# Kernel tuning notes

Hardware: AMD Instinct MI355X
Metric: run time of the kernel (lower is better)

Reference implementation:

```python
import jax, jax.numpy as jnp
import numpy as np

D_MODEL = 1024
N_HEAD = 16
DK = D_MODEL // N_HEAD
D_FF = 2048
EPS = 1e-6
NEG = -1e10


def layer_norm(x, gamma, beta):
    # torch .std() is unbiased (N-1), and eps is added to std (not var)
    mean = jnp.mean(x, axis=-1, keepdims=True)
    var = jnp.sum((x - mean) ** 2, axis=-1, keepdims=True) / (x.shape[-1] - 1)
    std = jnp.sqrt(var)
    return gamma * (x - mean) / (std + EPS) + beta


def setup_inputs() -> dict:
    key = jax.random.key(0)
    ks = jax.random.split(key, 12)
    s = 0.02
    inp = {
        'x': jax.random.normal(ks[0], (16, 512, D_MODEL), dtype=jnp.float32),
        'x_mask': jax.random.randint(ks[1], (16, 1, 1, 512), 0, 2, dtype=jnp.int32),
        'Wq': jax.random.normal(ks[2], (D_MODEL, D_MODEL), dtype=jnp.float32) * s,
        'bq': jnp.zeros((D_MODEL,), jnp.float32),
        'Wk': jax.random.normal(ks[3], (D_MODEL, D_MODEL), dtype=jnp.float32) * s,
        'bk': jnp.zeros((D_MODEL,), jnp.float32),
        'Wv': jax.random.normal(ks[4], (D_MODEL, D_MODEL), dtype=jnp.float32) * s,
        'bv': jnp.zeros((D_MODEL,), jnp.float32),
        'Wo': jax.random.normal(ks[5], (D_MODEL, D_MODEL), dtype=jnp.float32) * s,
        'bo': jnp.zeros((D_MODEL,), jnp.float32),
        'gamma1': jnp.ones((D_MODEL,), jnp.float32),
        'beta1': jnp.zeros((D_MODEL,), jnp.float32),
        'W1': jax.random.normal(ks[6], (D_MODEL, D_FF), dtype=jnp.float32) * s,
        'b1': jnp.zeros((D_FF,), jnp.float32),
        'W2': jax.random.normal(ks[7], (D_FF, D_MODEL), dtype=jnp.float32) * s,
        'b2': jnp.zeros((D_MODEL,), jnp.float32),
        'gamma2': jnp.ones((D_MODEL,), jnp.float32),
        'beta2': jnp.zeros((D_MODEL,), jnp.float32),
    }
    return inp


def reference(x, x_mask, Wq, bq, Wk, bk, Wv, bv, Wo, bo, gamma1, beta1,
              W1, b1, W2, b2, gamma2, beta2):
    B, S, _ = x.shape
    # QKV projections -> [B, S, H, DK]
    q = (x @ Wq + bq).reshape(B, S, N_HEAD, DK)
    k = (x @ Wk + bk).reshape(B, S, N_HEAD, DK)
    v = (x @ Wv + bv).reshape(B, S, N_HEAD, DK)
    # scores [B, H, Sq, Sk]
    scores = jnp.einsum('bqhd,bkhd->bhqk', q, k) / jnp.sqrt(jnp.float32(DK))
    scores = jnp.where(x_mask == 0, jnp.float32(NEG), scores)
    probs = jax.nn.softmax(scores, axis=-1)
    attn = jnp.einsum('bhqk,bkhd->bqhd', probs, v).reshape(B, S, D_MODEL)
    attn_out = attn @ Wo + bo
    # residual + post-LN 1
    h = layer_norm(attn_out + x, gamma1, beta1)
    # FFN (exact GELU as torch nn.GELU default)
    ffn = jax.nn.gelu(h @ W1 + b1, approximate=False) @ W2 + b2
    out = layer_norm(ffn + h, gamma2, beta2)
    return out
```

## Files before the change

### kernel.cpp

```cpp
#include <hip/hip_runtime.h>
#include <math.h>

#define B_ 16
#define S_ 512
#define DM 1024
#define NH 16
#define DFF 2048

typedef short bf16x8 __attribute__((ext_vector_type(8)));
typedef float f32x4 __attribute__((ext_vector_type(4)));
typedef unsigned short u16;

__device__ __forceinline__ u16 f2bf(float f) {
  unsigned int u = __float_as_uint(f);
  u += 0x7FFF + ((u >> 16) & 1);
  return (u16)(u >> 16);
}

__device__ __forceinline__ float bf2f(u16 u) {
  return __uint_as_float(((unsigned)u) << 16);
}

__device__ __forceinline__ unsigned cvtpk_bf16(float lo, float hi) {
  unsigned r;
  asm("v_cvt_pk_bf16_f32 %0, %1, %2" : "=v"(r) : "v"(lo), "v"(hi));
  return r;
}

__device__ __forceinline__ float gelu_exact(float x) {
  return 0.5f * x * (1.0f + erff(x * 0.70710678118654752f));
}

__device__ __forceinline__ void gload_lds16(const void* g, void* l) {
  __builtin_amdgcn_global_load_lds((const __attribute__((address_space(1))) void*)g,
                                   (__attribute__((address_space(3))) void*)l, 16, 0, 0);
}

#define QSCALE 0.18033688011112042f
#define MASKNEG -1.442695e10f


__global__ void cvt_bf16_k(const float* __restrict__ in, u16* __restrict__ out, int n) {
  int i = (blockIdx.x * blockDim.x + threadIdx.x) * 4;
  float4 v = *(const float4*)(in + i);
  uint2 pk;
  pk.x = (unsigned)f2bf(v.x) | ((unsigned)f2bf(v.y) << 16);
  pk.y = (unsigned)f2bf(v.z) | ((unsigned)f2bf(v.w) << 16);
  *(uint2*)(out + i) = pk;
}

__global__ void transpose_bf16(const float* __restrict__ W, u16* __restrict__ Wt, int K, int N) {
  __shared__ float tile[32][33];
  int n0 = blockIdx.x * 32, k0 = blockIdx.y * 32;
  int tx = threadIdx.x, ty = threadIdx.y;
#pragma unroll
  for (int j = 0; j < 32; j += 8)
    tile[ty + j][tx] = W[(size_t)(k0 + ty + j) * N + n0 + tx];
  __syncthreads();
#pragma unroll
  for (int j = 0; j < 32; j += 8)
    Wt[(size_t)(n0 + ty + j) * K + k0 + tx] = f2bf(tile[tx][ty + j]);
}

__global__ void bias_cat(const float* __restrict__ bq, const float* __restrict__ bk,
                         const float* __restrict__ bv, float* __restrict__ o) {
  int i = blockIdx.x * 256 + threadIdx.x;
  o[i] = (i < 1024) ? bq[i] : ((i < 2048) ? bk[i - 1024] : bv[i - 2048]);
}

template <int EPI>
__global__ __launch_bounds__(256, 2)
void gemm_mfma(const u16* __restrict__ A, const u16* __restrict__ Bt,
               const float* __restrict__ bias, void* __restrict__ Cout,
               u16* __restrict__ vT, int M, int N, int K) {
  __shared__ __align__(16) char lds[73728];
  const int tid = threadIdx.x;
  const int w = tid >> 6, lane = tid & 63;
  const int wm = w >> 1, wn = w & 1;

  const int gx = gridDim.x;
  const int nwg = gx * gridDim.y;
  const int lin = blockIdx.y * gx + blockIdx.x;
  const int wg = (lin & 7) * (nwg >> 3) + (lin >> 3);
  const int bm = wg / gx, bn = wg % gx;

  const int NT = K >> 5;

  const int srow = w * 16 + (lane >> 2);
  const int skel = ((lane & 3) ^ (lane >> 4)) * 8;
  const u16* gA = A + (size_t)(bm * 256 + srow) * K + skel;
  const u16* gB = Bt + (size_t)(bn * 128 + srow) * K + skel;
  const size_t rs64 = (size_t)64 * K;
  const int dstb = w * 1024;

  const int lr = lane & 15, kg = lane >> 4;
  const int kslot = (kg ^ ((lr >> 2) & 3)) << 4;
  const int fAoff = (wm * 128 + lr) * 64 + kslot;
  const int fBoff = 16384 + (wn * 64 + lr) * 64 + kslot;

  f32x4 acc[8][4];
#pragma unroll
  for (int i = 0; i < 8; ++i)
#pragma unroll
    for (int j = 0; j < 4; ++j) acc[i][j] = (f32x4){0.f, 0.f, 0.f, 0.f};

#define STAGE_A(t_, sl_)                                         \
  do {                                                           \
    const u16* g_ = gA + (size_t)(t_) * 32;                      \
    char* d_ = lds + (sl_) * 24576 + dstb;                       \
    gload_lds16(g_, d_);                                         \
    gload_lds16(g_ + rs64, d_ + 4096);                           \
    gload_lds16(g_ + 2 * rs64, d_ + 8192);                       \
    gload_lds16(g_ + 3 * rs64, d_ + 12288);                      \
  } while (0)
#define STAGE_B(t_, sl_)                                         \
  do {                                                           \
    const u16* g_ = gB + (size_t)(t_) * 32;                      \
    char* d_ = lds + (sl_) * 24576 + 16384 + dstb;               \
    gload_lds16(g_, d_);                                         \
    gload_lds16(g_ + rs64, d_ + 4096);                           \
  } while (0)

  STAGE_A(0, 0);
  STAGE_B(0, 0);
  STAGE_A(1, 1);
  STAGE_B(1, 1);
  asm volatile("s_waitcnt vmcnt(6)" ::: "memory");
  __builtin_amdgcn_s_barrier();
  __builtin_amdgcn_sched_barrier(0);

  int cs = 0, ss = 2;
  for (int t = 0; t < NT; ++t) {
    const int st = (t + 2 < NT) ? (t + 2) : (NT - 1);
    const char* fA = lds + cs * 24576 + fAoff;
    const char* fB = lds + cs * 24576 + fBoff;
    bf16x8 av[4], bv[4];
#pragma unroll
    for (int mi = 0; mi < 4; ++mi) av[mi] = *(const bf16x8*)(fA + mi * 1024);
#pragma unroll
    for (int ni = 0; ni < 4; ++ni) bv[ni] = *(const bf16x8*)(fB + ni * 1024);
    STAGE_A(st, ss);
    __builtin_amdgcn_s_setprio(1);
#pragma unroll
    for (int mi = 0; mi < 4; ++mi)
#pragma unroll
      for (int ni = 0; ni < 4; ++ni)
        acc[mi][ni] = __builtin_amdgcn_mfma_f32_16x16x32_bf16(av[mi], bv[ni], acc[mi][ni], 0, 0, 0);
    __builtin_amdgcn_s_setprio(0);
    bf16x8 av2[4];
#pragma unroll
    for (int mi = 0; mi < 4; ++mi) av2[mi] = *(const bf16x8*)(fA + 4096 + mi * 1024);
    STAGE_B(st, ss);
    __builtin_amdgcn_s_setprio(1);
#pragma unroll
    for (int mi = 0; mi < 4; ++mi)
#pragma unroll
      for (int ni = 0; ni < 4; ++ni)
        acc[4 + mi][ni] = __builtin_amdgcn_mfma_f32_16x16x32_bf16(av2[mi], bv[ni], acc[4 + mi][ni], 0, 0, 0);
    __builtin_amdgcn_s_setprio(0);
    asm volatile("s_waitcnt vmcnt(6) lgkmcnt(0)" ::: "memory");
    __builtin_amdgcn_s_barrier();
    __builtin_amdgcn_sched_barrier(0);
    cs = (cs == 2) ? 0 : cs + 1;
    ss = (ss == 2) ? 0 : ss + 1;
  }
#undef STAGE_A
#undef STAGE_B

  const int crow0 = bm * 256 + wm * 128;
  const int ccol0 = bn * 128 + wn * 64;
#pragma unroll
  for (int mi = 0; mi < 8; ++mi) {
#pragma unroll
    for (int ni = 0; ni < 4; ++ni) {
      const int col = ccol0 + ni * 16 + lr;
      const float bv = bias[col];
      const int rowb = crow0 + mi * 16 + (lane >> 4) * 4;
      float v[4];
#pragma unroll
      for (int r = 0; r < 4; ++r) v[r] = acc[mi][ni][r] + bv;
      if (EPI == 1) {
#pragma unroll
        for (int r = 0; r < 4; ++r)
          ((u16*)Cout)[(size_t)(rowb + r) * N + col] = f2bf(gelu_exact(v[r]));
      } else if (EPI == 2) {
#pragma unroll
        for (int r = 0; r < 4; ++r)
          ((float*)Cout)[(size_t)(rowb + r) * N + col] = v[r];
      } else if (EPI == 4) {
#pragma unroll
        for (int r = 0; r < 4; ++r)
          ((u16*)Cout)[(size_t)(rowb + r) * N + col] = f2bf(v[r]);
      } else {
        if (col < 2048) {
          const float sc = (col < 1024) ? QSCALE : 1.0f;
#pragma unroll
          for (int r = 0; r < 4; ++r)
            ((u16*)Cout)[(size_t)(rowb + r) * 2048 + col] = f2bf(v[r] * sc);
        } else {
          const int b = rowb >> 9, s = rowb & 511;
          const int hd = col - 2048;
          ushort4 pk;
          pk.x = f2bf(v[0]); pk.y = f2bf(v[1]); pk.z = f2bf(v[2]); pk.w = f2bf(v[3]);
          *(ushort4*)(vT + ((size_t)(b * NH + (hd >> 6)) * 64 + (hd & 63)) * S_ + s) = pk;
        }
      }
    }
  }
}

__global__ __launch_bounds__(256, 3)
void attn_kernel(const u16* __restrict__ qk,
                 const u16* __restrict__ vT,
                 const int* __restrict__ mask,
                 u16* __restrict__ out) {
  __shared__ __align__(16) u16 Qs[32 * 72];
  __shared__ __align__(16) u16 Pl[32 * 520];
  __shared__ __align__(16) float Mlf[512];
  __shared__ __align__(16) float Rsum[32][4];

  const int tid = threadIdx.x;
  const int w = tid >> 6, lane = tid & 63;
  const int bid = blockIdx.x;
  const int widx = (bid & 7) * 512 + (bid >> 3);
  const int qt = widx & 15, h = (widx >> 4) & 15, b = widx >> 8;
  const int q0 = qt * 32;
  const int arow = lane & 15, kg = lane >> 4;

  {
    int r = tid >> 3, slot = tid & 7;
    bf16x8 v = *(const bf16x8*)(qk + (size_t)(b * S_ + q0 + r) * 2048 + h * 64 + slot * 8);
    *(bf16x8*)((char*)Qs + r * 144 + slot * 16) = v;
  }
  Mlf[tid] = (mask[b * S_ + tid] == 0) ? MASKNEG : 0.f;
  Mlf[tid + 256] = (mask[b * S_ + tid + 256] == 0) ? MASKNEG : 0.f;

  const u16* vb = vT + ((size_t)(b * NH + h) * 64 + w * 16 + arow) * S_ + kg * 8;
  bf16x8 vv[8];
#pragma unroll
  for (int i = 0; i < 8; ++i) vv[i] = *(const bf16x8*)(vb + i * 32);

  __syncthreads();

  bf16x8 qf[2][2];
#pragma unroll
  for (int mi = 0; mi < 2; ++mi)
#pragma unroll
    for (int kk = 0; kk < 2; ++kk)
      qf[mi][kk] = *(const bf16x8*)((char*)Qs + (mi * 16 + arow) * 144 + kk * 64 + kg * 16);

  f32x4 s0[8], s1[8];
  const u16* kbase = qk + (size_t)(b * S_) * 2048 + 1024 + h * 64 + kg * 8;
#pragma unroll
  for (int half = 0; half < 2; ++half) {
    bf16x8 kvl[4][2];
#pragma unroll
    for (int j = 0; j < 4; ++j) {
      const int colg = w * 128 + (half * 4 + j) * 16 + arow;
      const u16* kr = kbase + (size_t)colg * 2048;
      kvl[j][0] = *(const bf16x8*)(kr);
      kvl[j][1] = *(const bf16x8*)(kr + 32);
    }
#pragma unroll
    for (int j = 0; j < 4; ++j) {
      const int ni = half * 4 + j;
      f32x4 a0 = {0.f, 0.f, 0.f, 0.f}, a1 = {0.f, 0.f, 0.f, 0.f};
      a0 = __builtin_amdgcn_mfma_f32_16x16x32_bf16(kvl[j][0], qf[0][0], a0, 0, 0, 0);
      a0 = __builtin_amdgcn_mfma_f32_16x16x32_bf16(kvl[j][1], qf[0][1], a0, 0, 0, 0);
      a1 = __builtin_amdgcn_mfma_f32_16x16x32_bf16(kvl[j][0], qf[1][0], a1, 0, 0, 0);
      a1 = __builtin_amdgcn_mfma_f32_16x16x32_bf16(kvl[j][1], qf[1][1], a1, 0, 0, 0);
      const f32x4 mb = *(const f32x4*)&Mlf[w * 128 + ni * 16 + kg * 4];
      s0[ni] = a0 + mb;
      s1[ni] = a1 + mb;
    }
  }

  f32x4 ac0 = {0.f, 0.f, 0.f, 0.f}, ac1 = ac0;
#pragma unroll
  for (int ni = 0; ni < 8; ++ni) {
#pragma unroll
    for (int r = 0; r < 4; ++r) {
      s0[ni][r] = __builtin_amdgcn_exp2f(s0[ni][r]);
      s1[ni][r] = __builtin_amdgcn_exp2f(s1[ni][r]);
    }
    ac0 += s0[ni];
    ac1 += s1[ni];
  }
  float t0 = ac0[0] + ac0[1] + ac0[2] + ac0[3];
  float t1 = ac1[0] + ac1[1] + ac1[2] + ac1[3];
  t0 += __shfl_xor(t0, 16);
  t0 += __shfl_xor(t0, 32);
  t1 += __shfl_xor(t1, 16);
  t1 += __shfl_xor(t1, 32);
  if (kg == 0) {
    Rsum[arow][w] = t0;
    Rsum[16 + arow][w] = t1;
  }

  {
    const int kq = w * 128 + kg * 4;
    char* const p0 = (char*)Pl + (arow * 520 + kq) * 2;
    char* const p1 = (char*)Pl + ((16 + arow) * 520 + kq) * 2;
#pragma unroll
    for (int ni = 0; ni < 8; ++ni) {
      uint2 pk;
      pk.x = cvtpk_bf16(s0[ni][0], s0[ni][1]);
      pk.y = cvtpk_bf16(s0[ni][2], s0[ni][3]);
      *(uint2*)(p0 + ni * 32) = pk;
      pk.x = cvtpk_bf16(s1[ni][0], s1[ni][1]);
      pk.y = cvtpk_bf16(s1[ni][2], s1[ni][3]);
      *(uint2*)(p1 + ni * 32) = pk;
    }
  }
  __syncthreads();

  {
    f32x4 oa[2];
    oa[0] = (f32x4){0.f, 0.f, 0.f, 0.f};
    oa[1] = (f32x4){0.f, 0.f, 0.f, 0.f};
#pragma unroll
    for (int t16 = 0; t16 < 16; ++t16) {
      const int sk0 = t16 * 32;
      bf16x8 bfr = (t16 < 8) ? vv[t16] : *(const bf16x8*)(vb + t16 * 32);
#pragma unroll
      for (int mi = 0; mi < 2; ++mi) {
        bf16x8 pa = *(const bf16x8*)(Pl + (mi * 16 + arow) * 520 + sk0 + kg * 8);
        oa[mi] = __builtin_amdgcn_mfma_f32_16x16x32_bf16(pa, bfr, oa[mi], 0, 0, 0);
      }
    }
#pragma unroll
    for (int mi = 0; mi < 2; ++mi)
#pragma unroll
      for (int r = 0; r < 4; ++r) {
        const int rloc = mi * 16 + kg * 4 + r;
        f32x4 sv = *(const f32x4*)&Rsum[rloc][0];
        const float inv = 1.0f / (sv[0] + sv[1] + sv[2] + sv[3]);
        const int qrow = q0 + rloc;
        out[(size_t)(b * S_ + qrow) * DM + h * 64 + w * 16 + arow] = f2bf(oa[mi][r] * inv);
      }
  }
}

template <int AB, int RB, int WF, int WB>
__global__ __launch_bounds__(256)
void ln_kernel(const void* __restrict__ a, const void* __restrict__ res,
               const float* __restrict__ gamma, const float* __restrict__ beta,
               float* __restrict__ outf, u16* __restrict__ outb) {
  const int row = blockIdx.x, tid = threadIdx.x;
  const int w = tid >> 6, lane = tid & 63;
  const size_t base = (size_t)row * DM + tid * 4;
  float v0, v1, v2, v3;
  {
    float a0, a1, a2, a3, r0, r1, r2, r3;
    if (AB) {
      ushort4 u = *(const ushort4*)((const u16*)a + base);
      a0 = bf2f(u.x); a1 = bf2f(u.y); a2 = bf2f(u.z); a3 = bf2f(u.w);
    } else {
      float4 u = *(const float4*)((const float*)a + base);
      a0 = u.x; a1 = u.y; a2 = u.z; a3 = u.w;
    }
    if (RB) {
      ushort4 u = *(const ushort4*)((const u16*)res + base);
      r0 = bf2f(u.x); r1 = bf2f(u.y); r2 = bf2f(u.z); r3 = bf2f(u.w);
    } else {
      float4 u = *(const float4*)((const float*)res + base);
      r0 = u.x; r1 = u.y; r2 = u.z; r3 = u.w;
    }
    v0 = a0 + r0; v1 = a1 + r1; v2 = a2 + r2; v3 = a3 + r3;
  }
  float s = v0 + v1 + v2 + v3;
  float ss = v0 * v0 + v1 * v1 + v2 * v2 + v3 * v3;
#pragma unroll
  for (int off = 32; off >= 1; off >>= 1) {
    s += __shfl_down(s, off);
    ss += __shfl_down(ss, off);
  }
  __shared__ float ps[4], pss[4], mb[2];
  if (lane == 0) { ps[w] = s; pss[w] = ss; }
  __syncthreads();
  if (tid == 0) {
    float S = ps[0] + ps[1] + ps[2] + ps[3];
    float SS = pss[0] + pss[1] + pss[2] + pss[3];
    float mean = S * (1.0f / DM);
    float var = (SS - (float)DM * mean * mean) * (1.0f / (DM - 1));
    var = fmaxf(var, 0.f);
    mb[0] = mean;
    mb[1] = 1.0f / (sqrtf(var) + 1e-6f);
  }
  __syncthreads();
  const float mean = mb[0], rinv = mb[1];
  const int c = tid * 4;
  float y0 = gamma[c] * (v0 - mean) * rinv + beta[c];
  float y1 = gamma[c + 1] * (v1 - mean) * rinv + beta[c + 1];
  float y2 = gamma[c + 2] * (v2 - mean) * rinv + beta[c + 2];
  float y3 = gamma[c + 3] * (v3 - mean) * rinv + beta[c + 3];
  if (WF) {
    float4 o = {y0, y1, y2, y3};
    *(float4*)(outf + base) = o;
  }
  if (WB) {
    uint2 pk;
    pk.x = (unsigned)f2bf(y0) | ((unsigned)f2bf(y1) << 16);
    pk.y = (unsigned)f2bf(y2) | ((unsigned)f2bf(y3) << 16);
    *(uint2*)(outb + base) = pk;
  }
}


extern "C" void kernel_launch(void* const* d_in, const int* in_sizes, int n_in,
                              void* d_out, int out_size, void* d_ws, size_t ws_size,
                              hipStream_t stream) {
  const float* x = (const float*)d_in[0];
  const int* xm = (const int*)d_in[1];
  const float* Wq = (const float*)d_in[2];
  const float* bq = (const float*)d_in[3];
  const float* Wk = (const float*)d_in[4];
  const float* bk = (const float*)d_in[5];
  const float* Wv = (const float*)d_in[6];
  const float* bv = (const float*)d_in[7];
  const float* Wo = (const float*)d_in[8];
  const float* bo = (const float*)d_in[9];
  const float* g1 = (const float*)d_in[10];
  const float* be1 = (const float*)d_in[11];
  const float* W1 = (const float*)d_in[12];
  const float* b1 = (const float*)d_in[13];
  const float* W2 = (const float*)d_in[14];
  const float* b2 = (const float*)d_in[15];
  const float* g2 = (const float*)d_in[16];
  const float* be2 = (const float*)d_in[17];

  char* ws = (char*)d_ws;
  u16* xb = (u16*)(ws);
  u16* wqkvt = (u16*)(ws + 16777216);
  u16* wot = (u16*)(ws + 23068672);
  u16* w1t = (u16*)(ws + 25165824);
  u16* w2t = (u16*)(ws + 29360128);
  float* bqkv = (float*)(ws + 33554432);
  u16* qkb = (u16*)(ws + 33566720);
  u16* vtb = (u16*)(ws + 67121152);
  u16* attnb = (u16*)(ws + 83898368);
  u16* attnpb = (u16*)(ws + 100675584);
  u16* f2b = (u16*)(ws + 117452800);
  u16* hb = xb;

  cvt_bf16_k<<<dim3(8192), dim3(256), 0, stream>>>(x, xb, 8388608);
  transpose_bf16<<<dim3(32, 32), dim3(32, 8), 0, stream>>>(Wq, wqkvt, 1024, 1024);
  transpose_bf16<<<dim3(32, 32), dim3(32, 8), 0, stream>>>(Wk, wqkvt + 1024 * 1024, 1024, 1024);
  transpose_bf16<<<dim3(32, 32), dim3(32, 8), 0, stream>>>(Wv, wqkvt + 2 * 1024 * 1024, 1024, 1024);
  transpose_bf16<<<dim3(32, 32), dim3(32, 8), 0, stream>>>(Wo, wot, 1024, 1024);
  transpose_bf16<<<dim3(64, 32), dim3(32, 8), 0, stream>>>(W1, w1t, 1024, 2048);
  transpose_bf16<<<dim3(32, 64), dim3(32, 8), 0, stream>>>(W2, w2t, 2048, 1024);
  bias_cat<<<dim3(12), dim3(256), 0, stream>>>(bq, bk, bv, bqkv);

  gemm_mfma<3><<<dim3(24, 32), dim3(256), 0, stream>>>(xb, wqkvt, bqkv, (void*)qkb, vtb, 8192, 3072, 1024);
  attn_kernel<<<dim3(4096), dim3(256), 0, stream>>>(qkb, vtb, xm, attnb);
  gemm_mfma<4><<<dim3(8, 32), dim3(256), 0, stream>>>(attnb, wot, bo, (void*)attnpb, (u16*)nullptr, 8192, 1024, 1024);
  ln_kernel<1, 0, 0, 1><<<dim3(8192), dim3(256), 0, stream>>>(attnpb, x, g1, be1, (float*)nullptr, hb);
  gemm_mfma<1><<<dim3(16, 32), dim3(256), 0, stream>>>(hb, w1t, b1, (void*)qkb, (u16*)nullptr, 8192, 2048, 1024);
  gemm_mfma<4><<<dim3(8, 32), dim3(256), 0, stream>>>(qkb, w2t, b2, (void*)f2b, (u16*)nullptr, 8192, 1024, 2048);
  ln_kernel<1, 1, 1, 0><<<dim3(8192), dim3(256), 0, stream>>>(f2b, hb, g2, be2, (float*)d_out, (u16*)nullptr);
}
```

Baseline: 305.9 us.

## Add 256x256 8-wave GEMM for QKV and FFN1; merge weight prep kernels

Adds a new 512-thread GEMM kernel with 256x256 output tiles and a triple-buffered LDS pipeline, used for the QKV projection and the first FFN GEMM. Larger tiles raise arithmetic intensity per block, cutting global and LDS traffic per FLOP. The six weight-transpose launches and the bias concat are also merged into one kernel to reduce launch overhead. The cost is more LDS per block (96KB) and fewer blocks in the grid, which may hurt occupancy or load balance.

```diff
diff --git a/kernel.cpp b/kernel.cpp
--- a/kernel.cpp
+++ b/kernel.cpp
@@ -49,10 +49,38 @@
   *(uint2*)(out + i) = pk;
 }
 
-__global__ void transpose_bf16(const float* __restrict__ W, u16* __restrict__ Wt, int K, int N) {
+__global__ __launch_bounds__(256)
+void prep_weights(const float* __restrict__ Wq, const float* __restrict__ Wk,
+                  const float* __restrict__ Wv, const float* __restrict__ Wo,
+                  const float* __restrict__ W1, const float* __restrict__ W2,
+                  u16* __restrict__ wqkvt, u16* __restrict__ wot,
+                  u16* __restrict__ w1t, u16* __restrict__ w2t,
+                  const float* __restrict__ bq, const float* __restrict__ bk,
+                  const float* __restrict__ bv, float* __restrict__ bqkv) {
+  const int bid = blockIdx.x;
+  if (bid >= 8192) {
+    int i = (bid - 8192) * 256 + threadIdx.x;
+    bqkv[i] = (i < 1024) ? bq[i] : ((i < 2048) ? bk[i - 1024] : bv[i - 2048]);
+    return;
+  }
+  const float* W;
+  u16* Wt;
+  int K, N, bx, by;
+  if (bid < 4096) {
+    const int m = bid >> 10, t = bid & 1023;
+    K = 1024; N = 1024; bx = t & 31; by = t >> 5;
+    W = (m == 0) ? Wq : (m == 1) ? Wk : (m == 2) ? Wv : Wo;
+    Wt = (m == 3) ? wot : wqkvt + m * 1048576;
+  } else if (bid < 6144) {
+    const int t = bid - 4096;
+    K = 1024; N = 2048; bx = t & 63; by = t >> 6; W = W1; Wt = w1t;
+  } else {
+    const int t = bid - 6144;
+    K = 2048; N = 1024; bx = t & 31; by = t >> 5; W = W2; Wt = w2t;
+  }
   __shared__ float tile[32][33];
-  int n0 = blockIdx.x * 32, k0 = blockIdx.y * 32;
-  int tx = threadIdx.x, ty = threadIdx.y;
+  const int n0 = bx * 32, k0 = by * 32;
+  const int tx = threadIdx.x & 31, ty = threadIdx.x >> 5;
 #pragma unroll
   for (int j = 0; j < 32; j += 8)
     tile[ty + j][tx] = W[(size_t)(k0 + ty + j) * N + n0 + tx];
@@ -62,17 +90,142 @@
     Wt[(size_t)(n0 + ty + j) * K + k0 + tx] = f2bf(tile[tx][ty + j]);
 }
 
-__global__ void bias_cat(const float* __restrict__ bq, const float* __restrict__ bk,
-                         const float* __restrict__ bv, float* __restrict__ o) {
-  int i = blockIdx.x * 256 + threadIdx.x;
-  o[i] = (i < 1024) ? bq[i] : ((i < 2048) ? bk[i - 1024] : bv[i - 2048]);
+template <int EPI>
+__global__ __launch_bounds__(512, 2)
+void gemm256(const u16* __restrict__ A, const u16* __restrict__ Bt,
+             const float* __restrict__ bias, void* __restrict__ Cout,
+             u16* __restrict__ vT, int M, int N, int K) {
+  __shared__ __align__(16) char lds[98304];
+  const int tid = threadIdx.x;
+  const int w = tid >> 6, lane = tid & 63;
+  const int wm = w >> 2, wn = w & 3;
+
+  const int gx = gridDim.x;
+  const int nwg = gx * gridDim.y;
+  const int lin = blockIdx.y * gx + blockIdx.x;
+  const int wg = (lin & 7) * (nwg >> 3) + (lin >> 3);
+  const int bm = wg / gx, bn = wg % gx;
+
+  const int NT = K >> 5;
+
+  const int srow = tid >> 2;
+  const int skel = ((tid & 3) ^ ((tid >> 4) & 3)) * 8;
+  const u16* gA = A + (size_t)(bm * 256 + srow) * K + skel;
+  const u16* gB = Bt + (size_t)(bn * 256 + srow) * K + skel;
+  const size_t rs128 = (size_t)128 * K;
+  const int dstb = w * 1024;
+
+  const int lr = lane & 15, kg = lane >> 4;
+  const int kslot = (kg ^ ((lr >> 2) & 3)) << 4;
+  const int fAoff = (wm * 128 + lr) * 64 + kslot;
+  const int fBoff = 16384 + (wn * 64 + lr) * 64 + kslot;
+
+  f32x4 acc[8][4];
+#pragma unroll
+  for (int i = 0; i < 8; ++i)
+#pragma unroll
+    for (int j = 0; j < 4; ++j) acc[i][j] = (f32x4){0.f, 0.f, 0.f, 0.f};
+
+#define STAGE_A(t_, sl_)                                   \
+  do {                                                     \
+    const u16* g_ = gA + (size_t)(t_) * 32;                \
+    char* d_ = lds + (sl_) * 32768 + dstb;                 \
+    gload_lds16(g_, d_);                                   \
+    gload_lds16(g_ + rs128, d_ + 8192);                    \
+  } while (0)
+#define STAGE_B(t_, sl_)                                   \
+  do {                                                     \
+    const u16* g_ = gB + (size_t)(t_) * 32;                \
+    char* d_ = lds + (sl_) * 32768 + 16384 + dstb;         \
+    gload_lds16(g_, d_);                                   \
+    gload_lds16(g_ + rs128, d_ + 8192);                    \
+  } while (0)
+
+  STAGE_A(0, 0);
+  STAGE_B(0, 0);
+  STAGE_A(1, 1);
+  STAGE_B(1, 1);
+  asm volatile("s_waitcnt vmcnt(4)" ::: "memory");
+  __builtin_amdgcn_s_barrier();
+  __builtin_amdgcn_sched_barrier(0);
+
+  int cs = 0, ss = 2;
+  for (int t = 0; t < NT; ++t) {
+    const int st = (t + 2 < NT) ? (t + 2) : (NT - 1);
+    const char* fA = lds + cs * 32768 + fAoff;
+    const char* fB = lds + cs * 32768 + fBoff;
+    bf16x8 av[4], bv[4];
+#pragma unroll
+    for (int mi = 0; mi < 4; ++mi) av[mi] = *(const bf16x8*)(fA + mi * 1024);
+#pragma unroll
+    for (int ni = 0; ni < 4; ++ni) bv[ni] = *(const bf16x8*)(fB + ni * 1024);
+    STAGE_A(st, ss);
+    __builtin_amdgcn_s_setprio(1);
+#pragma unroll
+    for (int mi = 0; mi < 4; ++mi)
+#pragma unroll
+      for (int ni = 0; ni < 4; ++ni)
+        acc[mi][ni] = __builtin_amdgcn_mfma_f32_16x16x32_bf16(av[mi], bv[ni], acc[mi][ni], 0, 0, 0);
+    __builtin_amdgcn_s_setprio(0);
+    bf16x8 av2[4];
+#pragma unroll
+    for (int mi = 0; mi < 4; ++mi) av2[mi] = *(const bf16x8*)(fA + 4096 + mi * 1024);
+    STAGE_B(st, ss);
+    __builtin_amdgcn_s_setprio(1);
+#pragma unroll
+    for (int mi = 0; mi < 4; ++mi)
+#pragma unroll
+      for (int ni = 0; ni < 4; ++ni)
+        acc[4 + mi][ni] = __builtin_amdgcn_mfma_f32_16x16x32_bf16(av2[mi], bv[ni], acc[4 + mi][ni], 0, 0, 0);
+    __builtin_amdgcn_s_setprio(0);
+    asm volatile("s_waitcnt vmcnt(4) lgkmcnt(0)" ::: "memory");
+    __builtin_amdgcn_s_barrier();
+    __builtin_amdgcn_sched_barrier(0);
+    cs = (cs == 2) ? 0 : cs + 1;
+    ss = (ss == 2) ? 0 : ss + 1;
+  }
+#undef STAGE_A
+#undef STAGE_B
+
+  const int crow0 = bm * 256 + wm * 128;
+  const int ccol0 = bn * 256 + wn * 64;
+#pragma unroll
+  for (int mi = 0; mi < 8; ++mi) {
+#pragma unroll
+    for (int ni = 0; ni < 4; ++ni) {
+      const int col = ccol0 + ni * 16 + lr;
+      const float bv = bias[col];
+      const int rowb = crow0 + mi * 16 + (lane >> 4) * 4;
+      float v[4];
+#pragma unroll
+      for (int r = 0; r < 4; ++r) v[r] = acc[mi][ni][r] + bv;
+      if (EPI == 1) {
+#pragma unroll
+        for (int r = 0; r < 4; ++r)
+          ((u16*)Cout)[(size_t)(rowb + r) * N + col] = f2bf(gelu_exact(v[r]));
+      } else {
+        if (col < 2048) {
+          const float sc = (col < 1024) ? QSCALE : 1.0f;
+#pragma unroll
+          for (int r = 0; r < 4; ++r)
+            ((u16*)Cout)[(size_t)(rowb + r) * 2048 + col] = f2bf(v[r] * sc);
+        } else {
+          const int b = rowb >> 9, s = rowb & 511;
+          const int hd = col - 2048;
+          ushort4 pk;
+          pk.x = f2bf(v[0]); pk.y = f2bf(v[1]); pk.z = f2bf(v[2]); pk.w = f2bf(v[3]);
+          *(ushort4*)(vT + ((size_t)(b * NH + (hd >> 6)) * 64 + (hd & 63)) * S_ + s) = pk;
+        }
+      }
+    }
+  }
 }
 
 template <int EPI>
 __global__ __launch_bounds__(256, 2)
 void gemm_mfma(const u16* __restrict__ A, const u16* __restrict__ Bt,
                const float* __restrict__ bias, void* __restrict__ Cout,
-               u16* __restrict__ vT, int M, int N, int K) {
+               int M, int N, int K) {
   __shared__ __align__(16) char lds[73728];
   const int tid = threadIdx.x;
   const int w = tid >> 6, lane = tid & 63;
@@ -176,35 +329,9 @@
       const int col = ccol0 + ni * 16 + lr;
       const float bv = bias[col];
       const int rowb = crow0 + mi * 16 + (lane >> 4) * 4;
-      float v[4];
-#pragma unroll
-      for (int r = 0; r < 4; ++r) v[r] = acc[mi][ni][r] + bv;
-      if (EPI == 1) {
-#pragma unroll
-        for (int r = 0; r < 4; ++r)
-          ((u16*)Cout)[(size_t)(rowb + r) * N + col] = f2bf(gelu_exact(v[r]));
-      } else if (EPI == 2) {
-#pragma unroll
-        for (int r = 0; r < 4; ++r)
-          ((float*)Cout)[(size_t)(rowb + r) * N + col] = v[r];
-      } else if (EPI == 4) {
-#pragma unroll
-        for (int r = 0; r < 4; ++r)
-          ((u16*)Cout)[(size_t)(rowb + r) * N + col] = f2bf(v[r]);
-      } else {
-        if (col < 2048) {
-          const float sc = (col < 1024) ? QSCALE : 1.0f;
-#pragma unroll
-          for (int r = 0; r < 4; ++r)
-            ((u16*)Cout)[(size_t)(rowb + r) * 2048 + col] = f2bf(v[r] * sc);
-        } else {
-          const int b = rowb >> 9, s = rowb & 511;
-          const int hd = col - 2048;
-          ushort4 pk;
-          pk.x = f2bf(v[0]); pk.y = f2bf(v[1]); pk.z = f2bf(v[2]); pk.w = f2bf(v[3]);
-          *(ushort4*)(vT + ((size_t)(b * NH + (hd >> 6)) * 64 + (hd & 63)) * S_ + s) = pk;
-        }
-      }
+#pragma unroll
+      for (int r = 0; r < 4; ++r)
+        ((u16*)Cout)[(size_t)(rowb + r) * N + col] = f2bf(acc[mi][ni][r] + bv);
     }
   }
 }
@@ -444,19 +571,15 @@
   u16* hb = xb;
 
   cvt_bf16_k<<<dim3(8192), dim3(256), 0, stream>>>(x, xb, 8388608);
-  transpose_bf16<<<dim3(32, 32), dim3(32, 8), 0, stream>>>(Wq, wqkvt, 1024, 1024);
-  transpose_bf16<<<dim3(32, 32), dim3(32, 8), 0, stream>>>(Wk, wqkvt + 1024 * 1024, 1024, 1024);
-  transpose_bf16<<<dim3(32, 32), dim3(32, 8), 0, stream>>>(Wv, wqkvt + 2 * 1024 * 1024, 1024, 1024);
-  transpose_bf16<<<dim3(32, 32), dim3(32, 8), 0, stream>>>(Wo, wot, 1024, 1024);
-  transpose_bf16<<<dim3(64, 32), dim3(32, 8), 0, stream>>>(W1, w1t, 1024, 2048);
-  transpose_bf16<<<dim3(32, 64), dim3(32, 8), 0, stream>>>(W2, w2t, 2048, 1024);
-  bias_cat<<<dim3(12), dim3(256), 0, stream>>>(bq, bk, bv, bqkv);
-
-  gemm_mfma<3><<<dim3(24, 32), dim3(256), 0, stream>>>(xb, wqkvt, bqkv, (void*)qkb, vtb, 8192, 3072, 1024);
+  prep_weights<<<dim3(8204), dim3(256), 0, stream>>>(Wq, Wk, Wv, Wo, W1, W2,
+                                                     wqkvt, wot, w1t, w2t,
+                                                     bq, bk, bv, bqkv);
+
+  gemm256<3><<<dim3(12, 32), dim3(512), 0, stream>>>(xb, wqkvt, bqkv, (void*)qkb, vtb, 8192, 3072, 1024);
   attn_kernel<<<dim3(4096), dim3(256), 0, stream>>>(qkb, vtb, xm, attnb);
-  gemm_mfma<4><<<dim3(8, 32), dim3(256), 0, stream>>>(attnb, wot, bo, (void*)attnpb, (u16*)nullptr, 8192, 1024, 1024);
+  gemm_mfma<4><<<dim3(8, 32), dim3(256), 0, stream>>>(attnb, wot, bo, (void*)attnpb, 8192, 1024, 1024);
   ln_kernel<1, 0, 0, 1><<<dim3(8192), dim3(256), 0, stream>>>(attnpb, x, g1, be1, (float*)nullptr, hb);
-  gemm_mfma<1><<<dim3(16, 32), dim3(256), 0, stream>>>(hb, w1t, b1, (void*)qkb, (u16*)nullptr, 8192, 2048, 1024);
-  gemm_mfma<4><<<dim3(8, 32), dim3(256), 0, stream>>>(qkb, w2t, b2, (void*)f2b, (u16*)nullptr, 8192, 1024, 2048);
+  gemm256<1><<<dim3(8, 32), dim3(512), 0, stream>>>(hb, w1t, b1, (void*)qkb, (u16*)nullptr, 8192, 2048, 1024);
+  gemm_mfma<4><<<dim3(8, 32), dim3(256), 0, stream>>>(qkb, w2t, b2, (void*)f2b, 8192, 1024, 2048);
   ln_kernel<1, 1, 1, 0><<<dim3(8192), dim3(256), 0, stream>>>(f2b, hb, g2, be2, (float*)d_out, (u16*)nullptr);
 }
```

Result: faster. 295.9 us (-3.3%).
